# Performance work log

Hardware: AMD Instinct MI355X
Metric: run time of the kernel (lower is better)

The kernel has to match this reference:

```python
import jax, jax.numpy as jnp
import numpy as np

BS = 2_000_000
FEAT = 22  # x(3) + R(9) + v(3) + w(3) + u(4)

# Constant physical parameters baked into the module's forward
_M = 1.0 / 0.027                      # inverse mass (Crazyflie, 0.027 kg)
_J = np.diag([2.3951e-05, 2.3951e-05, 3.2347e-05])  # inertia
M1_INV = jnp.asarray(_M * np.eye(3), dtype=jnp.float32)          # M_q_inv1
M2_INV = jnp.asarray(np.linalg.inv(_J), dtype=jnp.float32)       # M_q_inv2
M1 = jnp.asarray(np.linalg.inv(_M * np.eye(3)), dtype=jnp.float32)
M2 = jnp.asarray(_J, dtype=jnp.float32)
MG = jnp.float32(0.027 * 9.81)        # m*g, coefficient of V(q) = m*g*z


def setup_inputs() -> dict:
    key = jax.random.key(0)
    x = jax.random.normal(key, (BS, FEAT), dtype=jnp.float32)
    return {"t": 0, "input": x}


def reference(t, input):
    # split state
    R = input[:, 3:12]
    qdv = input[:, 12:15]   # linear velocity
    qdw = input[:, 15:18]   # angular velocity
    u = input[:, 18:22]     # control

    # momenta: p = M * q_dot  (M = inv(M_q_inv)); matmul(M, v) == v @ M.T
    pv = qdv @ M1.T
    pw = qdw @ M2.T

    # H = pv^T M1inv pv / 2 + pw^T M2inv pw / 2 + m*g*z.
    # H is quadratic in p with SYMMETRIC M_inv and linear in x, so the
    # autograd.grad in the original has the closed form:
    #   dHdpv = M1_inv pv,  dHdpw = M2_inv pw,  dHdx = (0,0,m*g),  dHdR = 0
    dHdpv = pv @ M1_INV.T
    dHdpw = pw @ M2_INV.T

    Rmat = R.reshape(-1, 3, 3)

    dx = jnp.einsum('bij,bj->bi', Rmat, dHdpv)
    dR = jnp.concatenate([
        jnp.cross(Rmat[:, 0, :], dHdpw),
        jnp.cross(Rmat[:, 1, :], dHdpw),
        jnp.cross(Rmat[:, 2, :], dHdpw),
    ], axis=1)

    # F = g_q @ u with g_q = [[0;0],[I4]] row layout -> F = (0, 0, u0, u1, u2, u3)
    Fv = jnp.concatenate([jnp.zeros_like(u[:, :2]), u[:, 0:1]], axis=1)
    Fw = u[:, 1:4]

    # R^T dHdx with dHdx = (0,0,mg) is mg * (third row of R)
    dpv = jnp.cross(pv, dHdpw) - MG * Rmat[:, 2, :] + Fv
    # dHdR = 0 so the cross(R_row, dHdR) terms vanish exactly
    dpw = jnp.cross(pw, dHdpw) + jnp.cross(pv, dHdpv) + Fw

    dv = dpv @ M1_INV.T
    dw = dpw @ M2_INV.T

    return jnp.concatenate([dx, dR, dv, dw, jnp.zeros_like(u)], axis=1)
```

## Files before the change

kernel.cpp:

```cpp
#include <hip/hip_runtime.h>

#define RPB 256

__global__ __launch_bounds__(RPB) void se3_ham_kernel(
    const float* __restrict__ in, float* __restrict__ out, int n_rows) {
    __shared__ float s[RPB * 22];

    const int block_row = blockIdx.x * RPB;
    int count = n_rows - block_row;
    if (count > RPB) count = RPB;
    if (count <= 0) return;
    const int nf  = count * 22;
    const int nf4 = nf >> 2;

    const float*  gin  = in + (size_t)block_row * 22;
    const float4* gin4 = (const float4*)gin;
    float4* s4 = (float4*)s;
    for (int i = threadIdx.x; i < nf4; i += RPB) s4[i] = gin4[i];
    for (int i = (nf4 << 2) + threadIdx.x; i < nf; i += RPB) s[i] = gin[i];
    __syncthreads();

    const int t = threadIdx.x;
    const bool active = (t < count);
    float o[22];
    if (active) {
        const float* p = &s[t * 22];
        const float R00=p[3],  R01=p[4],  R02=p[5];
        const float R10=p[6],  R11=p[7],  R12=p[8];
        const float R20=p[9],  R21=p[10], R22=p[11];
        const float qv0=p[12], qv1=p[13], qv2=p[14];
        const float qw0=p[15], qw1=p[16], qw2=p[17];
        const float u0 =p[18], u1 =p[19], u2 =p[20], u3=p[21];

        const float M1d   = (float)(1.0 / (1.0 / 0.027));
        const float Minv  = (float)(1.0 / 0.027);
        const float Jx    = (float)2.3951e-05;
        const float Jz    = (float)3.2347e-05;
        const float Jxinv = (float)(1.0 / 2.3951e-05);
        const float Jzinv = (float)(1.0 / 3.2347e-05);
        const float MG    = (float)(0.027 * 9.81);

        const float pv0 = M1d * qv0, pv1 = M1d * qv1, pv2 = M1d * qv2;
        const float pw0 = Jx * qw0,  pw1 = Jx * qw1,  pw2 = Jz * qw2;
        const float hv0 = Minv * pv0, hv1 = Minv * pv1, hv2 = Minv * pv2;
        const float hw0 = Jxinv * pw0, hw1 = Jxinv * pw1, hw2 = Jzinv * pw2;

        o[0] = R00*hv0 + R01*hv1 + R02*hv2;
        o[1] = R10*hv0 + R11*hv1 + R12*hv2;
        o[2] = R20*hv0 + R21*hv1 + R22*hv2;

        o[3]  = R01*hw2 - R02*hw1;  o[4]  = R02*hw0 - R00*hw2;  o[5]  = R00*hw1 - R01*hw0;
        o[6]  = R11*hw2 - R12*hw1;  o[7]  = R12*hw0 - R10*hw2;  o[8]  = R10*hw1 - R11*hw0;
        o[9]  = R21*hw2 - R22*hw1;  o[10] = R22*hw0 - R20*hw2;  o[11] = R20*hw1 - R21*hw0;

        const float dpv0 = (pv1*hw2 - pv2*hw1) - MG*R20;
        const float dpv1 = (pv2*hw0 - pv0*hw2) - MG*R21;
        const float dpv2 = (pv0*hw1 - pv1*hw0) - MG*R22 + u0;
        const float dpw0 = (pw1*hw2 - pw2*hw1) + (pv1*hv2 - pv2*hv1) + u1;
        const float dpw1 = (pw2*hw0 - pw0*hw2) + (pv2*hv0 - pv0*hv2) + u2;
        const float dpw2 = (pw0*hw1 - pw1*hw0) + (pv0*hv1 - pv1*hv0) + u3;

        o[12] = Minv * dpv0;  o[13] = Minv * dpv1;  o[14] = Minv * dpv2;
        o[15] = Jxinv * dpw0; o[16] = Jxinv * dpw1; o[17] = Jzinv * dpw2;

        o[18] = 0.0f; o[19] = 0.0f; o[20] = 0.0f; o[21] = 0.0f;
    }
    __syncthreads();

    if (active) {
        float* q = &s[t * 22];
        #pragma unroll
        for (int k = 0; k < 22; ++k) q[k] = o[k];
    }
    __syncthreads();

    float*  gout  = out + (size_t)block_row * 22;
    float4* gout4 = (float4*)gout;
    for (int i = threadIdx.x; i < nf4; i += RPB) gout4[i] = s4[i];
    for (int i = (nf4 << 2) + threadIdx.x; i < nf; i += RPB) gout[i] = s[i];
}

extern "C" void kernel_launch(void* const* d_in, const int* in_sizes, int n_in,
                              void* d_out, int out_size, void* d_ws, size_t ws_size,
                              hipStream_t stream) {
    const float* x = (const float*)d_in[1];
    float* y = (float*)d_out;
    const int n_rows = in_sizes[1] / 22;
    const int blocks = (n_rows + RPB - 1) / RPB;
    se3_ham_kernel<<<blocks, RPB, 0, stream>>>(x, y, n_rows);
}
```

Before: 301.0 us.

## Stage rows per wavefront with wave barriers and nontemporal loads/stores

Each 64-lane wavefront now stages its own 64 rows in a private slice of shared memory, replacing the three block-wide __syncthreads with wave-level barriers. Results are written back in place into the staging buffer, which removes the per-thread register copy and one barrier. Global loads and stores use nontemporal builtins to avoid polluting the cache on this streaming kernel. Relying on wave_barrier for LDS ordering assumes wave-synchronous execution and correct waitcnt insertion by the compiler.

```diff
diff --git a/kernel.cpp b/kernel.cpp
--- a/kernel.cpp
+++ b/kernel.cpp
@@ -1,30 +1,35 @@
 #include <hip/hip_runtime.h>
 
 #define RPB 256
+
+typedef float fvec4 __attribute__((ext_vector_type(4)));
 
 __global__ __launch_bounds__(RPB) void se3_ham_kernel(
     const float* __restrict__ in, float* __restrict__ out, int n_rows) {
     __shared__ float s[RPB * 22];
 
-    const int block_row = blockIdx.x * RPB;
-    int count = n_rows - block_row;
-    if (count > RPB) count = RPB;
-    if (count <= 0) return;
+    const int wave = threadIdx.x >> 6;
+    const int lane = threadIdx.x & 63;
+    const int row0 = blockIdx.x * RPB + (wave << 6);
+    if (row0 >= n_rows) return;
+    int count = n_rows - row0;
+    if (count > 64) count = 64;
     const int nf  = count * 22;
     const int nf4 = nf >> 2;
 
-    const float*  gin  = in + (size_t)block_row * 22;
-    const float4* gin4 = (const float4*)gin;
-    float4* s4 = (float4*)s;
-    for (int i = threadIdx.x; i < nf4; i += RPB) s4[i] = gin4[i];
-    for (int i = (nf4 << 2) + threadIdx.x; i < nf; i += RPB) s[i] = gin[i];
-    __syncthreads();
+    float* const sw = s + wave * (64 * 22);
+    fvec4* const s4 = (fvec4*)sw;
 
-    const int t = threadIdx.x;
-    const bool active = (t < count);
-    float o[22];
-    if (active) {
-        const float* p = &s[t * 22];
+    const float* gin  = in + (size_t)row0 * 22;
+    const fvec4* gin4 = (const fvec4*)gin;
+    for (int i = lane; i < nf4; i += 64)
+        s4[i] = __builtin_nontemporal_load(&gin4[i]);
+    for (int i = (nf4 << 2) + lane; i < nf; i += 64)
+        sw[i] = __builtin_nontemporal_load(&gin[i]);
+    __builtin_amdgcn_wave_barrier();
+
+    if (lane < count) {
+        float* p = &sw[lane * 22];
         const float R00=p[3],  R01=p[4],  R02=p[5];
         const float R10=p[6],  R11=p[7],  R12=p[8];
         const float R20=p[9],  R21=p[10], R22=p[11];
@@ -45,14 +50,6 @@
         const float hv0 = Minv * pv0, hv1 = Minv * pv1, hv2 = Minv * pv2;
         const float hw0 = Jxinv * pw0, hw1 = Jxinv * pw1, hw2 = Jzinv * pw2;
 
-        o[0] = R00*hv0 + R01*hv1 + R02*hv2;
-        o[1] = R10*hv0 + R11*hv1 + R12*hv2;
-        o[2] = R20*hv0 + R21*hv1 + R22*hv2;
-
-        o[3]  = R01*hw2 - R02*hw1;  o[4]  = R02*hw0 - R00*hw2;  o[5]  = R00*hw1 - R01*hw0;
-        o[6]  = R11*hw2 - R12*hw1;  o[7]  = R12*hw0 - R10*hw2;  o[8]  = R10*hw1 - R11*hw0;
-        o[9]  = R21*hw2 - R22*hw1;  o[10] = R22*hw0 - R20*hw2;  o[11] = R20*hw1 - R21*hw0;
-
         const float dpv0 = (pv1*hw2 - pv2*hw1) - MG*R20;
         const float dpv1 = (pv2*hw0 - pv0*hw2) - MG*R21;
         const float dpv2 = (pv0*hw1 - pv1*hw0) - MG*R22 + u0;
@@ -60,24 +57,27 @@
         const float dpw1 = (pw2*hw0 - pw0*hw2) + (pv2*hv0 - pv0*hv2) + u2;
         const float dpw2 = (pw0*hw1 - pw1*hw0) + (pv0*hv1 - pv1*hv0) + u3;
 
-        o[12] = Minv * dpv0;  o[13] = Minv * dpv1;  o[14] = Minv * dpv2;
-        o[15] = Jxinv * dpw0; o[16] = Jxinv * dpw1; o[17] = Jzinv * dpw2;
+        p[0] = R00*hv0 + R01*hv1 + R02*hv2;
+        p[1] = R10*hv0 + R11*hv1 + R12*hv2;
+        p[2] = R20*hv0 + R21*hv1 + R22*hv2;
 
-        o[18] = 0.0f; o[19] = 0.0f; o[20] = 0.0f; o[21] = 0.0f;
+        p[3]  = R01*hw2 - R02*hw1;  p[4]  = R02*hw0 - R00*hw2;  p[5]  = R00*hw1 - R01*hw0;
+        p[6]  = R11*hw2 - R12*hw1;  p[7]  = R12*hw0 - R10*hw2;  p[8]  = R10*hw1 - R11*hw0;
+        p[9]  = R21*hw2 - R22*hw1;  p[10] = R22*hw0 - R20*hw2;  p[11] = R20*hw1 - R21*hw0;
+
+        p[12] = Minv * dpv0;  p[13] = Minv * dpv1;  p[14] = Minv * dpv2;
+        p[15] = Jxinv * dpw0; p[16] = Jxinv * dpw1; p[17] = Jzinv * dpw2;
+
+        p[18] = 0.0f; p[19] = 0.0f; p[20] = 0.0f; p[21] = 0.0f;
     }
-    __syncthreads();
+    __builtin_amdgcn_wave_barrier();
 
-    if (active) {
-        float* q = &s[t * 22];
-        #pragma unroll
-        for (int k = 0; k < 22; ++k) q[k] = o[k];
-    }
-    __syncthreads();
-
-    float*  gout  = out + (size_t)block_row * 22;
-    float4* gout4 = (float4*)gout;
-    for (int i = threadIdx.x; i < nf4; i += RPB) gout4[i] = s4[i];
-    for (int i = (nf4 << 2) + threadIdx.x; i < nf; i += RPB) gout[i] = s[i];
+    float* gout  = out + (size_t)row0 * 22;
+    fvec4* gout4 = (fvec4*)gout;
+    for (int i = lane; i < nf4; i += 64)
+        __builtin_nontemporal_store(s4[i], &gout4[i]);
+    for (int i = (nf4 << 2) + lane; i < nf; i += 64)
+        gout[i] = sw[i];
 }
 
 extern "C" void kernel_launch(void* const* d_in, const int* in_sizes, int n_in,
```

Measured after the change: 288.4 us. 1.04x faster.
